# Optimization experiments

Measured on AMD Instinct MI355X. Metric: run time of the kernel, lower is better.

The kernel has to match this reference:

```python
import jax, jax.numpy as jnp
import numpy as np

D_MODEL = 1024
D_INNER = 2048      # expand=2 * d_model
HEADDIM = 64
NHEADS = D_INNER // HEADDIM   # 32 (ssm heads)
D_STATE = 128
D_CONV = 4
CHUNK = 256
D_IN_PROJ = 2 * D_INNER + 2 * D_STATE + NHEADS
CONV_DIM = D_INNER + 2 * D_STATE


def setup_inputs() -> dict:
    key = jax.random.key(0)
    ks = jax.random.split(key, 8)
    sc = lambda f: 1.0 / np.sqrt(f)
    dt_init = jax.random.uniform(ks[3], (NHEADS,), minval=0.001, maxval=0.1)
    return {
        "x": jax.random.normal(ks[0], (2, 4096, D_MODEL), jnp.float32),
        "W_in": jax.random.normal(ks[1], (D_MODEL, D_IN_PROJ), jnp.float32) * sc(D_MODEL),
        "conv_w": jax.random.normal(ks[2], (CONV_DIM, D_CONV), jnp.float32) * sc(D_CONV),
        "conv_b": jnp.zeros((CONV_DIM,), jnp.float32),
        "dt_bias": jnp.log(jnp.expm1(dt_init)),            # inverse softplus
        "A_log": jnp.log(jax.random.uniform(ks[4], (NHEADS,), minval=1.0, maxval=16.0)),
        "D": jnp.ones((NHEADS,), jnp.float32),
        "norm_w": jnp.ones((D_INNER,), jnp.float32),
        "W_out": jax.random.normal(ks[5], (D_INNER, D_MODEL), jnp.float32) * sc(D_INNER),
    }


def _segsum(a):
    # a: (..., T) -> (..., T, T) lower-triangular segment sums, -inf above diag
    T = a.shape[-1]
    cs = jnp.cumsum(a, axis=-1)
    diff = cs[..., :, None] - cs[..., None, :]
    mask = jnp.tril(jnp.ones((T, T), bool))
    return jnp.where(mask, diff, -jnp.inf)


def _ssd(x, A, B, C):
    # x: (b,L,h,p) already scaled by dt; A: (b,L,h) = dt*A_head; B,C: (b,L,n)
    b, L, h, p = x.shape
    nc = L // CHUNK
    xc = x.reshape(b, nc, CHUNK, h, p)
    Ac = A.reshape(b, nc, CHUNK, h).transpose(0, 3, 1, 2)      # (b,h,nc,cl)
    Bc = B.reshape(b, nc, CHUNK, -1)
    Cc = C.reshape(b, nc, CHUNK, -1)
    Acs = jnp.cumsum(Ac, axis=-1)
    # intra-chunk (diagonal) term
    Ldec = jnp.exp(_segsum(Ac))                                # (b,h,nc,cl,cl)
    Yd = jnp.einsum('bcln,bcsn,bhcls,bcshp->bclhp', Cc, Bc, Ldec, xc)
    # chunk end states
    decay_states = jnp.exp(Acs[..., -1:] - Acs)                # (b,h,nc,cl)
    states = jnp.einsum('bcln,bhcl,bclhp->bchpn', Bc, decay_states, xc)
    # inter-chunk recurrence (zero initial state)
    states = jnp.concatenate([jnp.zeros_like(states[:, :1]), states], axis=1)
    A_chunk = jnp.pad(Acs[..., -1], ((0, 0), (0, 0), (1, 0)))  # (b,h,nc+1)
    decay_chunk = jnp.exp(_segsum(A_chunk))                    # (b,h,nc+1,nc+1)
    states = jnp.einsum('bhzc,bchpn->bzhpn', decay_chunk, states)[:, :-1]
    # state -> output term
    out_decay = jnp.exp(Acs)                                   # (b,h,nc,cl)
    Yo = jnp.einsum('bcln,bchpn,bhcl->bclhp', Cc, states, out_decay)
    return (Yd + Yo).reshape(b, L, h, p)


def reference(x, W_in, conv_w, conv_b, dt_bias, A_log, D, norm_w, W_out):
    b, L, _ = x.shape
    zxbcdt = x @ W_in                                          # (b,L,4384)
    z, xBC, dt = jnp.split(zxbcdt, [D_INNER, 2 * D_INNER + 2 * D_STATE], axis=-1)
    # causal depthwise conv1d + silu
    xp = jnp.pad(xBC, ((0, 0), (D_CONV - 1, 0), (0, 0)))
    conv = sum(xp[:, k:k + L] * conv_w[:, k] for k in range(D_CONV)) + conv_b
    xBC = jax.nn.silu(conv)
    xs, B, C = jnp.split(xBC, [D_INNER, D_INNER + D_STATE], axis=-1)
    dt = jax.nn.softplus(dt + dt_bias)                         # (b,L,h)
    A = -jnp.exp(A_log)                                        # (h,)
    xh = xs.reshape(b, L, NHEADS, HEADDIM)
    y = _ssd(xh * dt[..., None], dt * A, B, C)                 # (b,L,h,p)
    y = y + xh * D[None, None, :, None]                        # D skip per head
    y = y.reshape(b, L, D_INNER)
    # gated RMSNorm
    u = y * jax.nn.silu(z)
    u = u * jax.lax.rsqrt(jnp.mean(u * u, axis=-1, keepdims=True) + 1e-5) * norm_w
    return u @ W_out
```

## Files before the change

### kernel.cpp

```cpp
#include <hip/hip_runtime.h>
#include <math.h>

#define B_ 2
#define L_ 4096
#define DM 1024
#define DI 2048
#define HD 64
#define NH 32
#define DS 128
#define CH 256
#define NC 16
#define DPROJ 4384
#define CONVD 2304
#define NGEMM 4352

typedef unsigned short u16;
typedef unsigned int u32;
typedef __attribute__((ext_vector_type(8))) short bf16x8;
typedef __attribute__((ext_vector_type(4))) float f32x4;

__device__ __forceinline__ float silu_(float x) { return x / (1.0f + __expf(-x)); }
__device__ __forceinline__ float us2f(u16 u) {
  union { u32 i; float f; } c; c.i = ((u32)u) << 16; return c.f;
}
__device__ __forceinline__ u16 f2us(float f) {
  union { float f; u32 i; } c; c.f = f;
  u32 i = c.i;
  return (u16)((i + 0x7FFFu + ((i >> 16) & 1u)) >> 16);
}
__device__ __forceinline__ void unpack8(uint4 v, float* o) {
  o[0] = us2f(v.x & 0xffffu); o[1] = us2f(v.x >> 16);
  o[2] = us2f(v.y & 0xffffu); o[3] = us2f(v.y >> 16);
  o[4] = us2f(v.z & 0xffffu); o[5] = us2f(v.z >> 16);
  o[6] = us2f(v.w & 0xffffu); o[7] = us2f(v.w >> 16);
}
__device__ __forceinline__ void unpk16(uint4 v, u16* o) {
  o[0] = (u16)(v.x & 0xffffu); o[1] = (u16)(v.x >> 16);
  o[2] = (u16)(v.y & 0xffffu); o[3] = (u16)(v.y >> 16);
  o[4] = (u16)(v.z & 0xffffu); o[5] = (u16)(v.z >> 16);
  o[6] = (u16)(v.w & 0xffffu); o[7] = (u16)(v.w >> 16);
}
__device__ __forceinline__ bf16x8 scale8(bf16x8 a, float s) {
  bf16x8 r;
#pragma unroll
  for (int j = 0; j < 8; ++j) r[j] = (short)f2us(us2f((u16)a[j]) * s);
  return r;
}
__device__ __forceinline__ void gload16(const u16* g, u16* l) {
  __builtin_amdgcn_global_load_lds(
      (const __attribute__((address_space(1))) void*)g,
      (__attribute__((address_space(3))) void*)l, 16, 0, 0);
}

__global__ __launch_bounds__(256) void cvt_t_k(const float* __restrict__ W,
                                               u16* __restrict__ Wt,
                                               int ldW, int ldT) {
  __shared__ float tile[64][65];
  const int t = threadIdx.x;
  const int n0 = blockIdx.x * 64, k0 = blockIdx.y * 64;
#pragma unroll
  for (int i = 0; i < 16; ++i) {
    int j = i * 256 + t;
    int kk = j >> 6, nn = j & 63;
    tile[kk][nn] = W[(size_t)(k0 + kk) * ldW + n0 + nn];
  }
  __syncthreads();
#pragma unroll
  for (int i = 0; i < 16; ++i) {
    int j = i * 256 + t;
    int nn = j >> 6, kk = j & 63;
    Wt[(size_t)(n0 + nn) * ldT + k0 + kk] = f2us(tile[kk][nn]);
  }
}

__global__ __launch_bounds__(512, 4) void gemm_in_k(const u16* __restrict__ A,
                                                    const u16* __restrict__ Bt,
                                                    u16* __restrict__ zb,
                                                    u16* __restrict__ xraw,
                                                    int nwg) {
  __shared__ u16 pool[24576];
  u16* Al = pool;
  u16* Bl = pool + 16384;
  const int t = threadIdx.x;
  const int w = t >> 6, lane = t & 63;
  const int fr = lane & 15, oct = lane >> 4;
  const int wm = w >> 1, wn = w & 1;
  const int q = nwg >> 3;
  const int wg = (blockIdx.x & 7) * q + (blockIdx.x >> 3);
  const int bm = wg / (NGEMM / 128), bn = wg % (NGEMM / 128);
  const int m0 = bm * 256, n0 = bn * 128;
  const int lr = lane >> 3, ls = lane & 7;
  const int gslot = (ls ^ lr) * 8;

  f32x4 acc[4][4];
#pragma unroll
  for (int mm = 0; mm < 4; ++mm)
#pragma unroll
    for (int nn = 0; nn < 4; ++nn) acc[mm][nn] = (f32x4){0.f, 0.f, 0.f, 0.f};

  for (int k0 = 0; k0 < DM; k0 += 64) {
    if (k0) __syncthreads();
#pragma unroll
    for (int i = 0; i < 4; ++i) {
      const int rowA = w * 32 + i * 8;
      gload16(&A[(size_t)(m0 + rowA + lr) * DM + k0 + gslot], &Al[rowA * 64]);
    }
#pragma unroll
    for (int i = 0; i < 2; ++i) {
      const int rowB = w * 16 + i * 8;
      gload16(&Bt[(size_t)(n0 + rowB + lr) * DM + k0 + gslot], &Bl[rowB * 64]);
    }
    __syncthreads();
#pragma unroll
    for (int kk = 0; kk < 2; ++kk) {
      bf16x8 af[4], bfr[4];
#pragma unroll
      for (int mm = 0; mm < 4; ++mm)
        af[mm] = *(const bf16x8*)&Al[(wm * 64 + mm * 16 + fr) * 64 +
                                     (((kk * 4 + oct) ^ (fr & 7)) * 8)];
#pragma unroll
      for (int nn = 0; nn < 4; ++nn)
        bfr[nn] = *(const bf16x8*)&Bl[(wn * 64 + nn * 16 + fr) * 64 +
                                      (((kk * 4 + oct) ^ (fr & 7)) * 8)];
      __builtin_amdgcn_s_setprio(1);
#pragma unroll
      for (int mm = 0; mm < 4; ++mm)
#pragma unroll
        for (int nn = 0; nn < 4; ++nn)
          acc[mm][nn] = __builtin_amdgcn_mfma_f32_16x16x32_bf16(af[mm], bfr[nn],
                                                                acc[mm][nn], 0, 0, 0);
      __builtin_amdgcn_s_setprio(0);
    }
  }

  const bool isz = (n0 < DI);
  u16* Oh = pool;
#pragma unroll
  for (int P = 0; P < 4; ++P) {
    __syncthreads();
    if (wm == P) {
#pragma unroll
      for (int mm = 0; mm < 4; ++mm)
#pragma unroll
        for (int i = 0; i < 4; ++i) {
          int rloc = mm * 16 + oct * 4 + i;
#pragma unroll
          for (int nn = 0; nn < 4; ++nn)
            Oh[rloc * 136 + wn * 64 + nn * 16 + fr] = f2us(acc[mm][nn][i]);
        }
    }
    __syncthreads();
#pragma unroll
    for (int p = 0; p < 2; ++p) {
      int e = p * 512 + t;
      int row = e >> 4, cs = (e & 15) * 8;
      uint4 v = *(const uint4*)&Oh[row * 136 + cs];
      size_t grow = m0 + P * 64 + row;
      int col = n0 + cs;
      if (isz) *(uint4*)&zb[grow * DI + col] = v;
      else     *(uint4*)&xraw[grow * CONVD + (col - DI)] = v;
    }
  }
}

template <int KDIM, int NTN>
__global__ __launch_bounds__(256) void gemm_bf16_k(const u16* __restrict__ A,
                                                   const u16* __restrict__ Bt,
                                                   float* __restrict__ outf,
                                                   int nwg) {
  __shared__ u16 pool[17408];
  u16* Al = pool;
  u16* Bl = pool + 8192;
  const int t = threadIdx.x;
  const int wv = t >> 6, lane = t & 63;
  const int fr = lane & 15, oct = lane >> 4;
  const int wr = wv >> 1, wc = wv & 1;
  const int q = nwg >> 3;
  const int wg = (blockIdx.x & 7) * q + (blockIdx.x >> 3);
  const int bm = wg / NTN, bn = wg % NTN;
  const int m0 = bm * 128, n0 = bn * 128;

  const int lr = lane >> 3, ls = lane & 7;
  const int gslot = (ls ^ lr) * 8;

  f32x4 acc[4][4];
#pragma unroll
  for (int mm = 0; mm < 4; ++mm)
#pragma unroll
    for (int nn = 0; nn < 4; ++nn) acc[mm][nn] = (f32x4){0.f, 0.f, 0.f, 0.f};

  for (int k0 = 0; k0 < KDIM; k0 += 64) {
    if (k0) __syncthreads();
#pragma unroll
    for (int i = 0; i < 4; ++i) {
      const int rowA = wv * 32 + i * 8;
      gload16(&A[(size_t)(m0 + rowA + lr) * KDIM + k0 + gslot], &Al[rowA * 64]);
      gload16(&Bt[(size_t)(n0 + rowA + lr) * KDIM + k0 + gslot], &Bl[rowA * 64]);
    }
    __syncthreads();
#pragma unroll
    for (int kk = 0; kk < 2; ++kk) {
      bf16x8 af[4], bfr[4];
#pragma unroll
      for (int mm = 0; mm < 4; ++mm)
        af[mm] = *(const bf16x8*)&Al[(wr * 64 + mm * 16 + fr) * 64 +
                                     (((kk * 4 + oct) ^ (fr & 7)) * 8)];
#pragma unroll
      for (int nn = 0; nn < 4; ++nn)
        bfr[nn] = *(const bf16x8*)&Bl[(wc * 64 + nn * 16 + fr) * 64 +
                                      (((kk * 4 + oct) ^ (fr & 7)) * 8)];
#pragma unroll
      for (int mm = 0; mm < 4; ++mm)
#pragma unroll
        for (int nn = 0; nn < 4; ++nn)
          acc[mm][nn] = __builtin_amdgcn_mfma_f32_16x16x32_bf16(af[mm], bfr[nn],
                                                                acc[mm][nn], 0, 0, 0);
    }
  }

#pragma unroll
  for (int P = 0; P < 2; ++P) {
    __syncthreads();
    float* Of = (float*)pool;
    if (wr == P) {
#pragma unroll
      for (int mm = 0; mm < 4; ++mm)
#pragma unroll
        for (int i = 0; i < 4; ++i) {
          int rloc = mm * 16 + oct * 4 + i;
#pragma unroll
          for (int nn = 0; nn < 4; ++nn)
            Of[rloc * 132 + wc * 64 + nn * 16 + fr] = acc[mm][nn][i];
        }
    }
    __syncthreads();
#pragma unroll
    for (int p = 0; p < 8; ++p) {
      int e = p * 256 + t;
      int row = e >> 5, c4 = (e & 31) * 4;
      float4 v = *(const float4*)&Of[row * 132 + c4];
      *(float4*)&outf[(size_t)(m0 + P * 64 + row) * DM + n0 + c4] = v;
    }
  }
}

__global__ __launch_bounds__(256) void dt_gemm_k(const float* __restrict__ x,
                                                 const float* __restrict__ W,
                                                 const float* __restrict__ dtb,
                                                 float* __restrict__ dtp,
                                                 u16* __restrict__ xb16) {
  __shared__ float xs[8 * 1024];
  const int t = threadIdx.x;
  const int row0 = blockIdx.x * 8;
#pragma unroll
  for (int i = 0; i < 8; ++i) {
    int j4 = i * 256 + t;
    float4 v = *(const float4*)&x[(size_t)row0 * DM + j4 * 4];
    *(float4*)&xs[j4 * 4] = v;
    u32 lo = (u32)f2us(v.x) | ((u32)f2us(v.y) << 16);
    u32 hi = (u32)f2us(v.z) | ((u32)f2us(v.w) << 16);
    *(uint2*)&xb16[(size_t)row0 * DM + j4 * 4] = make_uint2(lo, hi);
  }
  __syncthreads();
  const int r = t >> 5, h = t & 31;
  float a0 = 0.f, a1 = 0.f, a2 = 0.f, a3 = 0.f;
  const float* wcol = W + (DI + CONVD) + h;
  const float* xr = &xs[r * 1024];
  for (int k = 0; k < 1024; k += 4) {
    float4 xv = *(const float4*)&xr[k];
    a0 += xv.x * wcol[(size_t)(k + 0) * DPROJ];
    a1 += xv.y * wcol[(size_t)(k + 1) * DPROJ];
    a2 += xv.z * wcol[(size_t)(k + 2) * DPROJ];
    a3 += xv.w * wcol[(size_t)(k + 3) * DPROJ];
  }
  float v = (a0 + a1) + (a2 + a3) + dtb[h];
  dtp[(size_t)(row0 + r) * NH + h] = (v > 20.0f) ? v : log1pf(__expf(v));
}

__global__ __launch_bounds__(256) void conv_silu_k(const u16* __restrict__ xraw,
                                                   const float* __restrict__ cw,
                                                   const float* __restrict__ cb,
                                                   u16* __restrict__ xbc) {
  int idx = blockIdx.x * 256 + threadIdx.x;
  int ch8 = idx % (CONVD / 8);
  int bl = idx / (CONVD / 8);
  int l = bl & (L_ - 1);
  int ch = ch8 * 8;
  const u16* src = xraw + (size_t)bl * CONVD + ch;
  float a[8], o[8];
#pragma unroll
  for (int qq = 0; qq < 8; ++qq) a[qq] = cb[ch + qq];
  float w0[8], w1[8], w2[8], w3[8];
#pragma unroll
  for (int qq = 0; qq < 8; ++qq) {
    float4 w = *(const float4*)&cw[(ch + qq) * 4];
    w0[qq] = w.x; w1[qq] = w.y; w2[qq] = w.z; w3[qq] = w.w;
  }
  if (l >= 3) {
    uint4 v = *(const uint4*)&src[-3 * CONVD]; unpack8(v, o);
#pragma unroll
    for (int qq = 0; qq < 8; ++qq) a[qq] += o[qq] * w0[qq];
  }
  if (l >= 2) {
    uint4 v = *(const uint4*)&src[-2 * CONVD]; unpack8(v, o);
#pragma unroll
    for (int qq = 0; qq < 8; ++qq) a[qq] += o[qq] * w1[qq];
  }
  if (l >= 1) {
    uint4 v = *(const uint4*)&src[-CONVD]; unpack8(v, o);
#pragma unroll
    for (int qq = 0; qq < 8; ++qq) a[qq] += o[qq] * w2[qq];
  }
  {
    uint4 v = *(const uint4*)&src[0]; unpack8(v, o);
#pragma unroll
    for (int qq = 0; qq < 8; ++qq) a[qq] += o[qq] * w3[qq];
  }
  uint4 ov;
  ov.x = (u32)f2us(silu_(a[0])) | ((u32)f2us(silu_(a[1])) << 16);
  ov.y = (u32)f2us(silu_(a[2])) | ((u32)f2us(silu_(a[3])) << 16);
  ov.z = (u32)f2us(silu_(a[4])) | ((u32)f2us(silu_(a[5])) << 16);
  ov.w = (u32)f2us(silu_(a[6])) | ((u32)f2us(silu_(a[7])) << 16);
  *(uint4*)&xbc[(size_t)bl * CONVD + ch] = ov;
}

__global__ __launch_bounds__(256) void acs_k(const float* __restrict__ dtp,
                                             const float* __restrict__ A_log,
                                             float* __restrict__ Acs) {
  const int t = threadIdx.x;
  const int lane = t & 63, wv = t >> 6;
  const int idx = blockIdx.x * 4 + wv;
  const int h = (idx >> 4) & (NH - 1);
  const int c = idx & (NC - 1);
  const int b = idx >> 9;
  const float Ah = -__expf(A_log[h]);
  const size_t base = ((size_t)b * L_ + c * CH + lane * 4) * NH + h;
  float v0 = dtp[base] * Ah;
  float v1 = dtp[base + NH] * Ah;
  float v2 = dtp[base + 2 * NH] * Ah;
  float v3 = dtp[base + 3 * NH] * Ah;
  float c1 = v0 + v1, c2 = c1 + v2, c3 = c2 + v3;
  float tot = c3;
#pragma unroll
  for (int off = 1; off < 64; off <<= 1) {
    float p = __shfl_up(tot, off, 64);
    if (lane >= off) tot += p;
  }
  float excl = tot - c3;
  float4 ov = make_float4(excl + v0, excl + c1, excl + c2, excl + c3);
  *(float4*)&Acs[(size_t)idx * CH + lane * 4] = ov;
}

#define SLP 72
__global__ __launch_bounds__(256) void states_k(const u16* __restrict__ xbc,
                                                const float* __restrict__ dtp,
                                                const float* __restrict__ Acs,
                                                u16* __restrict__ st16) {
  __shared__ u16 BtT[128 * SLP];
  __shared__ u16 XtT[64 * SLP];
  const int t = threadIdx.x;
  const int wv = t >> 6, lane = t & 63;
  const int fr = lane & 15, oct = lane >> 4;
  const int sw = (blockIdx.x & 7) * 128 + (blockIdx.x >> 3);
  const int h = sw & 31, c = (sw >> 5) & 15, b = sw >> 9;
  const size_t acsb = (((size_t)b * NH + h) * NC + c) * CH;
  const float acs_last = Acs[acsb + (CH - 1)];
  const size_t rowbase = (size_t)b * L_ + c * CH;

  f32x4 acc[2][4];
#pragma unroll
  for (int mt = 0; mt < 2; ++mt)
#pragma unroll
    for (int pt = 0; pt < 4; ++pt) acc[mt][pt] = (f32x4){0.f, 0.f, 0.f, 0.f};

  for (int lt = 0; lt < 4; ++lt) {
    __syncthreads();
#pragma unroll
    for (int i = 0; i < 2; ++i) {
      int ci = i * 256 + t;
      int lp = ci >> 4, nk = ci & 15;
      int l0 = lp * 2;
      const u16* srcp = &xbc[(rowbase + lt * 64 + l0) * CONVD + DI + nk * 8];
      uint4 v0 = *(const uint4*)srcp;
      uint4 v1 = *(const uint4*)(srcp + CONVD);
      u16 a0[8], a1[8];
      unpk16(v0, a0); unpk16(v1, a1);
#pragma unroll
      for (int qq = 0; qq < 8; ++qq) {
        int r = nk * 8 + qq;
        u32 val = (u32)a0[qq] | ((u32)a1[qq] << 16);
        *(u32*)&BtT[r * SLP + ((((l0 >> 3) ^ (r >> 3)) & 7) << 3) + (l0 & 7)] = val;
      }
    }
    {
      int lp = t >> 3, pk = t & 7;
      int l0 = lp * 2;
      size_t row0 = rowbase + lt * 64 + l0;
      uint4 v0 = *(const uint4*)&xbc[row0 * CONVD + h * HD + pk * 8];
      uint4 v1 = *(const uint4*)&xbc[(row0 + 1) * CONVD + h * HD + pk * 8];
      float d0 = dtp[row0 * NH + h] * __expf(acs_last - Acs[acsb + lt * 64 + l0]);
      float d1 = dtp[(row0 + 1) * NH + h] * __expf(acs_last - Acs[acsb + lt * 64 + l0 + 1]);
      float o0[8], o1[8];
      unpack8(v0, o0); unpack8(v1, o1);
#pragma unroll
      for (int qq = 0; qq < 8; ++qq) {
        int r = pk * 8 + qq;
        u32 val = (u32)f2us(o0[qq] * d0) | ((u32)f2us(o1[qq] * d1) << 16);
        *(u32*)&XtT[r * SLP + ((((l0 >> 3) ^ (r >> 3)) & 7) << 3) + (l0 & 7)] = val;
      }
    }
    __syncthreads();
    __builtin_amdgcn_s_setprio(1);
#pragma unroll
    for (int ks = 0; ks < 2; ++ks) {
      bf16x8 afr[2], bfr[4];
#pragma unroll
      for (int mt = 0; mt < 2; ++mt) {
        int r = wv * 32 + mt * 16 + fr;
        afr[mt] = *(const bf16x8*)&BtT[r * SLP + ((((ks * 4 + oct) ^ (r >> 3)) & 7) << 3)];
      }
#pragma unroll
      for (int pt = 0; pt < 4; ++pt) {
        int r = pt * 16 + fr;
        bfr[pt] = *(const bf16x8*)&XtT[r * SLP + ((((ks * 4 + oct) ^ (r >> 3)) & 7) << 3)];
      }
#pragma unroll
      for (int mt = 0; mt < 2; ++mt)
#pragma unroll
        for (int pt = 0; pt < 4; ++pt)
          acc[mt][pt] = __builtin_amdgcn_mfma_f32_16x16x32_bf16(afr[mt], bfr[pt],
                                                                acc[mt][pt], 0, 0, 0);
    }
    __builtin_amdgcn_s_setprio(0);
  }
  size_t sbase = (((size_t)b * NC + c) * NH + h) * (size_t)(HD * DS);
#pragma unroll
  for (int mt = 0; mt < 2; ++mt)
#pragma unroll
    for (int pt = 0; pt < 4; ++pt) {
      int p = pt * 16 + fr;
      int n0 = wv * 32 + mt * 16 + oct * 4;
      u32 lo = (u32)f2us(acc[mt][pt][0]) | ((u32)f2us(acc[mt][pt][1]) << 16);
      u32 hi = (u32)f2us(acc[mt][pt][2]) | ((u32)f2us(acc[mt][pt][3]) << 16);
      *(uint2*)&st16[sbase + (size_t)p * DS + n0] = make_uint2(lo, hi);
    }
}

__global__ __launch_bounds__(256) void scan_k(u16* __restrict__ st16,
                                              const float* __restrict__ Acs) {
  const int t = threadIdx.x;
  const int seg = blockIdx.x & 15;
  const int bh = blockIdx.x >> 4;
  const int h = bh & 31, b = bh >> 5;
  const int e2 = seg * 256 + t;
  const size_t acssb = ((size_t)b * NH + h) * NC * CH;
  float run0 = 0.0f, run1 = 0.0f;
#pragma unroll
  for (int c = 0; c < NC; ++c) {
    float dAl = __expf(Acs[acssb + (size_t)c * CH + (CH - 1)]);
    size_t e = (((size_t)b * NC + c) * NH + h) * (size_t)(HD * DS) + e2 * 2;
    u32 v = *(const u32*)&st16[e];
    float s0 = us2f((u16)(v & 0xffffu)), s1 = us2f((u16)(v >> 16));
    *(u32*)&st16[e] = (u32)f2us(run0) | ((u32)f2us(run1) << 16);
    run0 = fmaf(dAl, run0, s0);
    run1 = fmaf(dAl, run1, s1);
  }
}

#define SP 72
#define XOFF 8192
#define POFF 12800
__global__ __launch_bounds__(512, 4) void ssd_out_k(const u16* __restrict__ xbc,
                                                    const float* __restrict__ dtp,
                                                    const float* __restrict__ Acs,
                                                    const u16* __restrict__ st16,
                                                    const float* __restrict__ Dvec,
                                                    u16* __restrict__ y) {
  __shared__ u16 pool[31232];
  __shared__ float acs_s[256];
  const int t = threadIdx.x;
  const int w = t >> 6, lane = t & 63;
  const int fr = lane & 15, oct = lane >> 4;
  const int sw = (blockIdx.x & 7) * 128 + (blockIdx.x >> 3);
  const int h = sw & 31, c = (sw >> 5) & 15, b = sw >> 9;
  const size_t acsb = (((size_t)b * NH + h) * NC + c) * CH;
  const size_t rowbase = (size_t)b * L_ + c * CH;
  if (t < 256) acs_s[t] = Acs[acsb + t];
  const size_t sb = (((size_t)b * NC + c) * NH + h) * (size_t)(HD * DS);
#pragma unroll
  for (int i = 0; i < 2; ++i) {
    int ci = i * 512 + t; int p = ci >> 4, nk = ci & 15;
    uint4 v = *(const uint4*)&st16[sb + (size_t)p * DS + nk * 8];
    *(uint4*)&pool[p * 136 + nk * 8] = v;
  }
  __syncthreads();
  bf16x8 ca[2][4];
#pragma unroll
  for (int mt = 0; mt < 2; ++mt)
#pragma unroll
    for (int kk = 0; kk < 4; ++kk)
      ca[mt][kk] = *(const bf16x8*)&xbc[(rowbase + w * 32 + mt * 16 + fr) * CONVD +
                                        DI + DS + kk * 32 + oct * 8];
  f32x4 acc_y[2][4];
#pragma unroll
  for (int mt = 0; mt < 2; ++mt)
#pragma unroll
    for (int pp4 = 0; pp4 < 4; ++pp4) acc_y[mt][pp4] = (f32x4){0.f, 0.f, 0.f, 0.f};

  {
    float eL0 = __expf(acs_s[w * 32 + fr]);
    float eL1 = __expf(acs_s[w * 32 + 16 + fr]);
    __builtin_amdgcn_s_setprio(1);
#pragma unroll
    for (int kk = 0; kk < 4; ++kk) {
      bf16x8 c0 = scale8(ca[0][kk], eL0);
      bf16x8 c1 = scale8(ca[1][kk], eL1);
#pragma unroll
      for (int pp4 = 0; pp4 < 4; ++pp4) {
        bf16x8 sf = *(const bf16x8*)&pool[(pp4 * 16 + fr) * 136 + kk * 32 + oct * 8];
        acc_y[0][pp4] = __builtin_amdgcn_mfma_f32_16x16x32_bf16(c0, sf, acc_y[0][pp4], 0, 0, 0);
        acc_y[1][pp4] = __builtin_amdgcn_mfma_f32_16x16x32_bf16(c1, sf, acc_y[1][pp4], 0, 0, 0);
      }
    }
    __builtin_amdgcn_s_setprio(0);
  }

  const int stmax = w >> 1, delta = (w & 1) << 5;
  for (int st = 0; st < 4; ++st) {
    __syncthreads();
#pragma unroll
    for (int i = 0; i < 2; ++i) {
      int ci = i * 512 + t; int ll = ci >> 4, ck = ci & 15;
      uint4 v = *(const uint4*)&xbc[(rowbase + st * 64 + ll) * CONVD + DI + ck * 8];
      *(uint4*)&pool[ll * 128 + ((ck * 8) ^ ((ll & 7) << 3))] = v;
    }
    if (t < 256) {
      int lp = t >> 3, pk = t & 7;
      int s0 = lp * 2;
      size_t row0 = rowbase + st * 64 + s0;
      uint4 v0 = *(const uint4*)&xbc[row0 * CONVD + h * HD + pk * 8];
      uint4 v1 = *(const uint4*)&xbc[(row0 + 1) * CONVD + h * HD + pk * 8];
      float d0 = dtp[row0 * NH + h];
      float d1 = dtp[(row0 + 1) * NH + h];
      float o0[8], o1[8];
      unpack8(v0, o0); unpack8(v1, o1);
#pragma unroll
      for (int qq = 0; qq < 8; ++qq) {
        int r = pk * 8 + qq;
        u32 val = (u32)f2us(o0[qq] * d0) | ((u32)f2us(o1[qq] * d1) << 16);
        *(u32*)&pool[XOFF + r * SP + ((((s0 >> 3) ^ (r >> 3)) & 7) << 3) + (s0 & 7)] = val;
      }
    }
    __syncthreads();
    if (st > stmax) continue;
    const bool diag = (st == stmax);
#pragma unroll
    for (int ss4 = 0; ss4 < 4; ++ss4) {
      bf16x8 bbf[4];
#pragma unroll
      for (int kk = 0; kk < 4; ++kk)
        bbf[kk] = *(const bf16x8*)&pool[(ss4 * 16 + fr) * 128 +
                                        ((kk * 32 + oct * 8) ^ ((fr & 7) << 3))];
      int s_in = ss4 * 16 + fr;
      float aS = acs_s[st * 64 + s_in];
#pragma unroll
      for (int mt = 0; mt < 2; ++mt) {
        f32x4 sacc = (f32x4){0.f, 0.f, 0.f, 0.f};
        __builtin_amdgcn_s_setprio(1);
#pragma unroll
        for (int kk = 0; kk < 4; ++kk)
          sacc = __builtin_amdgcn_mfma_f32_16x16x32_bf16(ca[mt][kk], bbf[kk], sacc, 0, 0, 0);
        __builtin_amdgcn_s_setprio(0);
#pragma unroll
        for (int i = 0; i < 4; ++i) {
          int r = mt * 16 + oct * 4 + i;
          float aL = acs_s[w * 32 + r];
          float wgt = (!diag || (s_in <= r + delta)) ? __expf(aL - aS) : 0.0f;
          pool[POFF + w * 2304 + r * SP + s_in] = f2us(sacc[i] * wgt);
        }
      }
    }
    bf16x8 pa[2][2];
#pragma unroll
    for (int mt = 0; mt < 2; ++mt)
#pragma unroll
      for (int k2 = 0; k2 < 2; ++k2)
        pa[mt][k2] = *(const bf16x8*)&pool[POFF + w * 2304 + (mt * 16 + fr) * SP +
                                           k2 * 32 + oct * 8];
    __builtin_amdgcn_s_setprio(1);
#pragma unroll
    for (int pp4 = 0; pp4 < 4; ++pp4) {
      int rx = pp4 * 16 + fr, xg = rx >> 3;
      bf16x8 xb0 = *(const bf16x8*)&pool[XOFF + rx * SP + (((oct) ^ xg) & 7) * 8];
      bf16x8 xb1 = *(const bf16x8*)&pool[XOFF + rx * SP + (((4 + oct) ^ xg) & 7) * 8];
#pragma unroll
      for (int mt = 0; mt < 2; ++mt) {
        acc_y[mt][pp4] = __builtin_amdgcn_mfma_f32_16x16x32_bf16(pa[mt][0], xb0, acc_y[mt][pp4], 0, 0, 0);
        acc_y[mt][pp4] = __builtin_amdgcn_mfma_f32_16x16x32_bf16(pa[mt][1], xb1, acc_y[mt][pp4], 0, 0, 0);
      }
    }
    __builtin_amdgcn_s_setprio(0);
  }

  const float Dh = Dvec[h];
#pragma unroll
  for (int mt = 0; mt < 2; ++mt)
#pragma unroll
    for (int i = 0; i < 4; ++i) {
      size_t row = rowbase + w * 32 + mt * 16 + oct * 4 + i;
#pragma unroll
      for (int pp4 = 0; pp4 < 4; ++pp4) {
        int col = h * HD + pp4 * 16 + fr;
        float xs = us2f(xbc[row * CONVD + col]);
        y[row * DI + col] = f2us(acc_y[mt][pp4][i] + Dh * xs);
      }
    }
}

__global__ __launch_bounds__(256) void gnorm_k(const u16* __restrict__ zb,
                                               const float* __restrict__ nw,
                                               u16* __restrict__ y) {
  const int row = blockIdx.x, t = threadIdx.x;
  const u16* zr = zb + (size_t)row * DI;
  u16* yr = y + (size_t)row * DI;
  uint4 zv = *(const uint4*)&zr[t * 8];
  uint4 yv = *(const uint4*)&yr[t * 8];
  float uz[8], uy[8];
  unpack8(zv, uz); unpack8(yv, uy);
  float u[8], ssum = 0.0f;
#pragma unroll
  for (int j = 0; j < 8; ++j) { u[j] = uy[j] * silu_(uz[j]); ssum += u[j] * u[j]; }
#pragma unroll
  for (int off = 32; off >= 1; off >>= 1) ssum += __shfl_xor(ssum, off, 64);
  __shared__ float red[4];
  if ((t & 63) == 0) red[t >> 6] = ssum;
  __syncthreads();
  float sc = rsqrtf((red[0] + red[1] + red[2] + red[3]) * (1.0f / DI) + 1e-5f);
  float4 w0 = *(const float4*)&nw[t * 8];
  float4 w1 = *(const float4*)&nw[t * 8 + 4];
  float o0 = u[0] * sc * w0.x, o1 = u[1] * sc * w0.y, o2 = u[2] * sc * w0.z, o3 = u[3] * sc * w0.w;
  float o4 = u[4] * sc * w1.x, o5 = u[5] * sc * w1.y, o6 = u[6] * sc * w1.z, o7 = u[7] * sc * w1.w;
  uint4 ov;
  ov.x = (u32)f2us(o0) | ((u32)f2us(o1) << 16);
  ov.y = (u32)f2us(o2) | ((u32)f2us(o3) << 16);
  ov.z = (u32)f2us(o4) | ((u32)f2us(o5) << 16);
  ov.w = (u32)f2us(o6) | ((u32)f2us(o7) << 16);
  *(uint4*)&yr[t * 8] = ov;
}

extern "C" void kernel_launch(void* const* d_in, const int* in_sizes, int n_in,
                              void* d_out, int out_size, void* d_ws, size_t ws_size,
                              hipStream_t stream) {
  const float* x      = (const float*)d_in[0];
  const float* W_in   = (const float*)d_in[1];
  const float* conv_w = (const float*)d_in[2];
  const float* conv_b = (const float*)d_in[3];
  const float* dt_b   = (const float*)d_in[4];
  const float* A_log  = (const float*)d_in[5];
  const float* Dvec   = (const float*)d_in[6];
  const float* norm_w = (const float*)d_in[7];
  const float* W_out  = (const float*)d_in[8];
  float* out = (float*)d_out;

  u16* zb       = (u16*)d_ws;
  u16* xbc      = zb + (size_t)B_ * L_ * DI;
  float* dtp    = (float*)(xbc + (size_t)B_ * L_ * CONVD);
  float* Acs    = dtp + (size_t)B_ * L_ * NH;
  u16* stregion = (u16*)(Acs + (size_t)B_ * NH * L_);
  u16* uni      = stregion + (size_t)B_ * NC * NH * HD * DS * 2;
  u16* xraw = uni;
  u16* y    = uni;

  u16* xb16     = stregion;
  u16* wint     = stregion + (size_t)B_ * L_ * DM;
  u16* states16 = stregion;
  u16* woutt    = stregion;

  const int Mrows = B_ * L_;

  dt_gemm_k<<<Mrows / 8, 256, 0, stream>>>(x, W_in, dt_b, dtp, xb16);
  cvt_t_k<<<dim3(NGEMM / 64, DM / 64), 256, 0, stream>>>(W_in, wint, DPROJ, DM);

  const int nwg_in = (Mrows / 256) * (NGEMM / 128);
  gemm_in_k<<<nwg_in, 512, 0, stream>>>(xb16, wint, zb, xraw, nwg_in);

  conv_silu_k<<<(Mrows * (CONVD / 8)) / 256, 256, 0, stream>>>(xraw, conv_w, conv_b, xbc);
  acs_k<<<(B_ * NH * NC) / 4, 256, 0, stream>>>(dtp, A_log, Acs);
  states_k<<<B_ * NC * NH, 256, 0, stream>>>(xbc, dtp, Acs, states16);
  scan_k<<<B_ * NH * 16, 256, 0, stream>>>(states16, Acs);
  ssd_out_k<<<B_ * NC * NH, 512, 0, stream>>>(xbc, dtp, Acs, states16, Dvec, y);
  gnorm_k<<<Mrows, 256, 0, stream>>>(zb, norm_w, y);

  cvt_t_k<<<dim3(DM / 64, DI / 64), 256, 0, stream>>>(W_out, woutt, DM, DI);
  const int nwg_out = (Mrows / 128) * (DM / 128);
  gemm_bf16_k<DI, DM / 128><<<nwg_out, 256, 0, stream>>>(y, woutt, out, nwg_out);
}
```

Before: 345.9 us.

## Fuse gated RMSNorm into SSD output and out-projection epilogue

```diff
diff --git a/kernel.cpp b/kernel.cpp
--- a/kernel.cpp
+++ b/kernel.cpp
@@ -73,6 +73,28 @@
   }
 }
 
+__global__ __launch_bounds__(256) void cvt_tw_k(const float* __restrict__ W,
+                                                const float* __restrict__ nw,
+                                                u16* __restrict__ Wt,
+                                                int ldW, int ldT) {
+  __shared__ float tile[64][65];
+  const int t = threadIdx.x;
+  const int n0 = blockIdx.x * 64, k0 = blockIdx.y * 64;
+#pragma unroll
+  for (int i = 0; i < 16; ++i) {
+    int j = i * 256 + t;
+    int kk = j >> 6, nn = j & 63;
+    tile[kk][nn] = W[(size_t)(k0 + kk) * ldW + n0 + nn] * nw[k0 + kk];
+  }
+  __syncthreads();
+#pragma unroll
+  for (int i = 0; i < 16; ++i) {
+    int j = i * 256 + t;
+    int nn = j >> 6, kk = j & 63;
+    Wt[(size_t)(n0 + nn) * ldT + k0 + kk] = f2us(tile[kk][nn]);
+  }
+}
+
 __global__ __launch_bounds__(512, 4) void gemm_in_k(const u16* __restrict__ A,
                                                     const u16* __restrict__ Bt,
                                                     u16* __restrict__ zb,
@@ -166,6 +188,7 @@
 template <int KDIM, int NTN>
 __global__ __launch_bounds__(256) void gemm_bf16_k(const u16* __restrict__ A,
                                                    const u16* __restrict__ Bt,
+                                                   const float* __restrict__ rowsum,
                                                    float* __restrict__ outf,
                                                    int nwg) {
   __shared__ u16 pool[17408];
@@ -238,10 +261,26 @@
     for (int p = 0; p < 8; ++p) {
       int e = p * 256 + t;
       int row = e >> 5, c4 = (e & 31) * 4;
+      size_t grow = m0 + P * 64 + row;
+      float s = rsqrtf(rowsum[grow] * (1.0f / DI) + 1e-5f);
       float4 v = *(const float4*)&Of[row * 132 + c4];
-      *(float4*)&outf[(size_t)(m0 + P * 64 + row) * DM + n0 + c4] = v;
-    }
-  }
+      v.x *= s; v.y *= s; v.z *= s; v.w *= s;
+      *(float4*)&outf[grow * DM + n0 + c4] = v;
+    }
+  }
+}
+
+__global__ __launch_bounds__(256) void rowsum_k(const float* __restrict__ psum,
+                                                float* __restrict__ rowsum) {
+  int row = blockIdx.x * 256 + threadIdx.x;
+  const float4* p = (const float4*)&psum[(size_t)row * 32];
+  float s = 0.0f;
+#pragma unroll
+  for (int i = 0; i < 8; ++i) {
+    float4 v = p[i];
+    s += (v.x + v.y) + (v.z + v.w);
+  }
+  rowsum[row] = s;
 }
 
 __global__ __launch_bounds__(256) void dt_gemm_k(const float* __restrict__ x,
@@ -475,7 +514,9 @@
                                                     const float* __restrict__ Acs,
                                                     const u16* __restrict__ st16,
                                                     const float* __restrict__ Dvec,
-                                                    u16* __restrict__ y) {
+                                                    const u16* __restrict__ zb,
+                                                    u16* __restrict__ v_out,
+                                                    float* __restrict__ psum) {
   __shared__ u16 pool[31232];
   __shared__ float acs_s[256];
   const int t = threadIdx.x;
@@ -603,49 +644,36 @@
   }
 
   const float Dh = Dvec[h];
+  float rs[2][4];
 #pragma unroll
   for (int mt = 0; mt < 2; ++mt)
 #pragma unroll
     for (int i = 0; i < 4; ++i) {
       size_t row = rowbase + w * 32 + mt * 16 + oct * 4 + i;
+      float rsum = 0.0f;
 #pragma unroll
       for (int pp4 = 0; pp4 < 4; ++pp4) {
         int col = h * HD + pp4 * 16 + fr;
         float xs = us2f(xbc[row * CONVD + col]);
-        y[row * DI + col] = f2us(acc_y[mt][pp4][i] + Dh * xs);
-      }
-    }
-}
-
-__global__ __launch_bounds__(256) void gnorm_k(const u16* __restrict__ zb,
-                                               const float* __restrict__ nw,
-                                               u16* __restrict__ y) {
-  const int row = blockIdx.x, t = threadIdx.x;
-  const u16* zr = zb + (size_t)row * DI;
-  u16* yr = y + (size_t)row * DI;
-  uint4 zv = *(const uint4*)&zr[t * 8];
-  uint4 yv = *(const uint4*)&yr[t * 8];
-  float uz[8], uy[8];
-  unpack8(zv, uz); unpack8(yv, uy);
-  float u[8], ssum = 0.0f;
-#pragma unroll
-  for (int j = 0; j < 8; ++j) { u[j] = uy[j] * silu_(uz[j]); ssum += u[j] * u[j]; }
-#pragma unroll
-  for (int off = 32; off >= 1; off >>= 1) ssum += __shfl_xor(ssum, off, 64);
-  __shared__ float red[4];
-  if ((t & 63) == 0) red[t >> 6] = ssum;
-  __syncthreads();
-  float sc = rsqrtf((red[0] + red[1] + red[2] + red[3]) * (1.0f / DI) + 1e-5f);
-  float4 w0 = *(const float4*)&nw[t * 8];
-  float4 w1 = *(const float4*)&nw[t * 8 + 4];
-  float o0 = u[0] * sc * w0.x, o1 = u[1] * sc * w0.y, o2 = u[2] * sc * w0.z, o3 = u[3] * sc * w0.w;
-  float o4 = u[4] * sc * w1.x, o5 = u[5] * sc * w1.y, o6 = u[6] * sc * w1.z, o7 = u[7] * sc * w1.w;
-  uint4 ov;
-  ov.x = (u32)f2us(o0) | ((u32)f2us(o1) << 16);
-  ov.y = (u32)f2us(o2) | ((u32)f2us(o3) << 16);
-  ov.z = (u32)f2us(o4) | ((u32)f2us(o5) << 16);
-  ov.w = (u32)f2us(o6) | ((u32)f2us(o7) << 16);
-  *(uint4*)&yr[t * 8] = ov;
+        float zz = us2f(zb[row * DI + col]);
+        float vv = (acc_y[mt][pp4][i] + Dh * xs) * silu_(zz);
+        v_out[row * DI + col] = f2us(vv);
+        rsum += vv * vv;
+      }
+      rs[mt][i] = rsum;
+    }
+#pragma unroll
+  for (int mt = 0; mt < 2; ++mt)
+#pragma unroll
+    for (int i = 0; i < 4; ++i) {
+      float s = rs[mt][i];
+#pragma unroll
+      for (int off = 8; off >= 1; off >>= 1) s += __shfl_xor(s, off, 64);
+      if (fr == 0) {
+        size_t row = rowbase + w * 32 + mt * 16 + oct * 4 + i;
+        psum[row * 32 + h] = s;
+      }
+    }
 }
 
 extern "C" void kernel_launch(void* const* d_in, const int* in_sizes, int n_in,
@@ -669,11 +697,13 @@
   u16* stregion = (u16*)(Acs + (size_t)B_ * NH * L_);
   u16* uni      = stregion + (size_t)B_ * NC * NH * HD * DS * 2;
   u16* xraw = uni;
-  u16* y    = uni;
+  u16* v    = uni;
 
   u16* xb16     = stregion;
   u16* wint     = stregion + (size_t)B_ * L_ * DM;
   u16* states16 = stregion;
+  float* psum   = (float*)(stregion + (size_t)B_ * NC * NH * HD * DS);
+  float* rowsum = psum + (size_t)B_ * L_ * NH;
   u16* woutt    = stregion;
 
   const int Mrows = B_ * L_;
@@ -688,10 +718,11 @@
   acs_k<<<(B_ * NH * NC) / 4, 256, 0, stream>>>(dtp, A_log, Acs);
   states_k<<<B_ * NC * NH, 256, 0, stream>>>(xbc, dtp, Acs, states16);
   scan_k<<<B_ * NH * 16, 256, 0, stream>>>(states16, Acs);
-  ssd_out_k<<<B_ * NC * NH, 512, 0, stream>>>(xbc, dtp, Acs, states16, Dvec, y);
-  gnorm_k<<<Mrows, 256, 0, stream>>>(zb, norm_w, y);
-
-  cvt_t_k<<<dim3(DM / 64, DI / 64), 256, 0, stream>>>(W_out, woutt, DM, DI);
+  ssd_out_k<<<B_ * NC * NH, 512, 0, stream>>>(xbc, dtp, Acs, states16, Dvec,
+                                              zb, v, psum);
+  rowsum_k<<<Mrows / 256, 256, 0, stream>>>(psum, rowsum);
+
+  cvt_tw_k<<<dim3(DM / 64, DI / 64), 256, 0, stream>>>(W_out, norm_w, woutt, DM, DI);
   const int nwg_out = (Mrows / 128) * (DM / 128);
-  gemm_bf16_k<DI, DM / 128><<<nwg_out, 256, 0, stream>>>(y, woutt, out, nwg_out);
-}
+  gemm_bf16_k<DI, DM / 128><<<nwg_out, 256, 0, stream>>>(v, woutt, rowsum, out, nwg_out);
+}
```

Result: no change. 339.6 us (-1.8%).
